# Optimization experiments

Hardware: AMD Instinct MI355X
Metric: run time of the kernel (lower is better)

## Reference

```python
import jax, jax.numpy as jnp
import numpy as np

N = 1024
DIM = 128
HEADS = 8
DK = DIM // HEADS
EDIM = 16
EPS = 1e-5
NEG = -10000.0


def _lin(k, din, dout):
    return jax.random.normal(k, (din, dout), jnp.float32) * (1.0 / np.sqrt(din))


def setup_inputs() -> dict:
    key = jax.random.key(0)
    ks = jax.random.split(key, 10)
    mask = jax.random.randint(ks[2], (N, N), 0, 2).astype(bool)
    mask = mask | jnp.eye(N, dtype=bool)  # self-loops always valid
    return {
        "x": jax.random.normal(ks[0], (N, DIM), jnp.float32),
        "edge_feat": jax.random.normal(ks[1], (N, N, EDIM), jnp.float32),
        "mask": mask,
        "Wq": _lin(ks[3], DIM, DIM), "bq": jnp.zeros((DIM,), jnp.float32),
        "Wk": _lin(ks[4], DIM, DIM), "bk": jnp.zeros((DIM,), jnp.float32),
        "Wv": _lin(ks[5], DIM, DIM), "bv": jnp.zeros((DIM,), jnp.float32),
        "Wae": _lin(ks[6], EDIM, HEADS), "bae": jnp.zeros((HEADS,), jnp.float32),
        "Wve": _lin(ks[7], EDIM, DIM), "bve": jnp.zeros((DIM,), jnp.float32),
        "Wo": _lin(ks[8], DIM, DIM), "bo": jnp.zeros((DIM,), jnp.float32),
        "gamma": jnp.ones((DIM,), jnp.float32),
        "beta": jnp.zeros((DIM,), jnp.float32),
    }


def reference(x, edge_feat, mask, Wq, bq, Wk, bk, Wv, bv, Wae, bae, Wve, bve, Wo, bo, gamma, beta):
    n, dim = x.shape
    heads = bae.shape[0]
    dk = dim // heads
    # pre-LayerNorm
    mu = jnp.mean(x, axis=-1, keepdims=True)
    var = jnp.mean(jnp.square(x - mu), axis=-1, keepdims=True)
    h = (x - mu) * jax.lax.rsqrt(var + EPS) * gamma + beta
    q = (h @ Wq + bq).reshape(n, heads, dk)
    k = (h @ Wk + bk).reshape(n, heads, dk)
    v = (h @ Wv + bv).reshape(n, heads, dk)
    # attention logits with per-edge additive bias: (n, m, heads)
    att = jnp.einsum('nhd,mhd->nmh', q, k) / np.sqrt(dk).astype(np.float32)
    att = att + edge_feat @ Wae + bae
    att = jnp.where(mask[..., None], att, NEG)
    alpha = jax.nn.softmax(att, axis=1)  # softmax over source nodes m
    # edge-conditioned values: msg_{nm} = v_m + U(e_{nm})
    edge_val = (edge_feat @ Wve + bve).reshape(n, n, heads, dk)
    out = jnp.einsum('nmh,mhd->nhd', alpha, v) + jnp.einsum('nmh,nmhd->nhd', alpha, edge_val)
    out = out.reshape(n, dim) @ Wo + bo
    return x + out
```

## Files before the change

### kernel.cpp

```cpp
#include <hip/hip_runtime.h>
#include <hip/hip_bf16.h>

#define NNODE 1024
#define DIM 128
#define HEADS 8
#define DK 16
#define EDIM 16
#define BN 8
#define NGRP 8
#define KV_ROW 160
#define H_STRIDE 20
#define EF_ROW 20
#define EFW_NSTR 104
#define LOG2E 1.44269504f

#define WREG 2176
#define VW_OFF 640
#define EFW_OFF 1280
#define MKW_OFF 2112
#define SMEM_F (4 * WREG)

__global__ __launch_bounds__(384)
void ln_qkv_kernel(const float* __restrict__ x,
                   const float* __restrict__ Wq, const float* __restrict__ bq,
                   const float* __restrict__ Wk, const float* __restrict__ bk,
                   const float* __restrict__ Wv, const float* __restrict__ bv,
                   const float* __restrict__ gamma, const float* __restrict__ beta,
                   float* __restrict__ qg, float* __restrict__ kg, float* __restrict__ vg) {
    const int n = blockIdx.x;
    const int t = threadIdx.x;
    __shared__ float hrow[DIM];
    __shared__ float part[4];

    float xv = 0.f;
    if (t < 128) {
        xv = x[n * DIM + t];
        float v = xv;
        #pragma unroll
        for (int off = 32; off >= 1; off >>= 1) v += __shfl_xor(v, off);
        if ((t & 63) == 0) part[t >> 6] = v;
    }
    __syncthreads();
    const float mu = (part[0] + part[1]) * (1.0f / DIM);
    const float dx = xv - mu;
    if (t < 128) {
        float v = dx * dx;
        #pragma unroll
        for (int off = 32; off >= 1; off >>= 1) v += __shfl_xor(v, off);
        if ((t & 63) == 0) part[2 + (t >> 6)] = v;
    }
    __syncthreads();
    if (t < 128) {
        const float var = (part[2] + part[3]) * (1.0f / DIM);
        hrow[t] = dx * rsqrtf(var + 1e-5f) * gamma[t] + beta[t];
    }
    __syncthreads();

    const int which = t >> 7;
    const int col = t & 127;
    const float* W = (which == 0) ? Wq : (which == 1) ? Wk : Wv;
    const float* b = (which == 0) ? bq : (which == 1) ? bk : bv;
    float* o       = (which == 0) ? qg : (which == 1) ? kg : vg;
    float a0 = b[col], a1 = 0.f;
    #pragma unroll 8
    for (int i = 0; i < DIM; i += 2) {
        a0 = fmaf(hrow[i],     W[i * DIM + col],       a0);
        a1 = fmaf(hrow[i + 1], W[(i + 1) * DIM + col], a1);
    }
    o[n * DIM + col] = a0 + a1;
}

__global__ __launch_bounds__(256, 2)
void attn_kernel(const float* __restrict__ qg, const float* __restrict__ kg,
                 const float* __restrict__ vg, const float* __restrict__ ef,
                 const int* __restrict__ mask,
                 const float* __restrict__ Wae, const float* __restrict__ bae,
                 float* __restrict__ acc) {
    const int t = threadIdx.x;
    const int lane = t & 63;
    const int wid = t >> 6;
    const int sp = lane >> 5;
    const int np = (lane >> 3) & 3;
    const int h  = lane & 7;
    const int bx = blockIdx.x;
    const int n0  = (bx >> 3) * BN;
    const int grp = bx & 7;
    const int mb_w = grp * 128 + wid * 32;

    __shared__ float smem[SMEM_F];
    float* k_w  = smem + wid * WREG;
    float* v_w  = k_w + VW_OFF;
    float* ef_w = k_w + EFW_OFF;
    int*   mk_w = (int*)(k_w + MKW_OFF);

    float qreg[2][DK];
    #pragma unroll
    for (int hf = 0; hf < 2; ++hf) {
        const float* qp = qg + (size_t)(n0 + np + 4 * hf) * DIM + h * DK;
        #pragma unroll
        for (int d4 = 0; d4 < 4; ++d4) {
            const float4 qv = *(const float4*)(qp + d4 * 4);
            qreg[hf][d4 * 4 + 0] = qv.x; qreg[hf][d4 * 4 + 1] = qv.y;
            qreg[hf][d4 * 4 + 2] = qv.z; qreg[hf][d4 * 4 + 3] = qv.w;
        }
    }
    float waec[EDIM];
    #pragma unroll
    for (int e = 0; e < EDIM; ++e) waec[e] = Wae[e * HEADS + h] * LOG2E;
    const float baeh = bae[h] * LOG2E;

    float sl[2] = {0.f, 0.f};
    float accv[2][DK], accT[2][EDIM];
    #pragma unroll
    for (int hf = 0; hf < 2; ++hf) {
        #pragma unroll
        for (int d = 0; d < DK; ++d) accv[hf][d] = 0.f;
        #pragma unroll
        for (int e = 0; e < EDIM; ++e) accT[hf][e] = 0.f;
    }

    #pragma unroll 1
    for (int c = 0; c < 8; ++c) {
        const int mb = mb_w + c * 4;

        const int kvrow = sp * 2 + (np >> 1);
        const int kvc4  = (np & 1) * 16 + (h << 1);
        float4 kq[2], vq[2], ev[2]; int mki = 0;
        #pragma unroll
        for (int r = 0; r < 2; ++r) {
            const int idx = r * 64 + lane;
            const int row = idx >> 5, c4 = idx & 31;
            kq[r] = *(const float4*)(kg + (size_t)(mb + row) * DIM + c4 * 4);
            vq[r] = *(const float4*)(vg + (size_t)(mb + row) * DIM + c4 * 4);
        }
        #pragma unroll
        for (int r = 0; r < 2; ++r) {
            const int idx = r * 64 + lane;
            const int nn = idx >> 4, mm = (idx >> 2) & 3, q4 = idx & 3;
            ev[r] = *(const float4*)(ef + ((size_t)(n0 + nn) * NNODE + mb + mm) * EDIM + q4 * 4);
        }
        if (lane < 32)
            mki = mask[(size_t)(n0 + (lane >> 2)) * NNODE + (mb + (lane & 3))];
        #pragma unroll
        for (int r = 0; r < 2; ++r) {
            const int idx = r * 64 + lane;
            const int row = idx >> 5, c4 = idx & 31;
            const int hh = c4 >> 2, d4 = c4 & 3;
            *(float4*)&k_w[row * KV_ROW + hh * H_STRIDE + d4 * 4] = kq[r];
            *(float4*)&v_w[row * KV_ROW + hh * H_STRIDE + d4 * 4] = vq[r];
        }
        #pragma unroll
        for (int r = 0; r < 2; ++r) {
            const int idx = r * 64 + lane;
            const int nn = idx >> 4, mm = (idx >> 2) & 3, q4 = idx & 3;
            *(float4*)&ef_w[nn * EFW_NSTR + mm * EF_ROW + q4 * 4] = ev[r];
        }
        if (lane < 32)
            mk_w[lane] = mki;

        #pragma unroll
        for (int j = 0; j < 2; ++j) {
            const int ml = sp * 2 + j;
            float kk[DK], vv[DK];
            const float* kp = &k_w[ml * KV_ROW + h * H_STRIDE];
            const float* vp = &v_w[ml * KV_ROW + h * H_STRIDE];
            #pragma unroll
            for (int d4 = 0; d4 < 4; ++d4) {
                const float4 k4 = *(const float4*)(kp + d4 * 4);
                kk[d4 * 4 + 0] = k4.x; kk[d4 * 4 + 1] = k4.y;
                kk[d4 * 4 + 2] = k4.z; kk[d4 * 4 + 3] = k4.w;
                const float4 v4 = *(const float4*)(vp + d4 * 4);
                vv[d4 * 4 + 0] = v4.x; vv[d4 * 4 + 1] = v4.y;
                vv[d4 * 4 + 2] = v4.z; vv[d4 * 4 + 3] = v4.w;
            }
            #pragma unroll
            for (int hf = 0; hf < 2; ++hf) {
                const int n = np + 4 * hf;
                const float* ep = &ef_w[n * EFW_NSTR + ml * EF_ROW];
                float efv[EDIM];
                #pragma unroll
                for (int e4 = 0; e4 < 4; ++e4) {
                    const float4 e4v = *(const float4*)(ep + e4 * 4);
                    efv[e4 * 4 + 0] = e4v.x; efv[e4 * 4 + 1] = e4v.y;
                    efv[e4 * 4 + 2] = e4v.z; efv[e4 * 4 + 3] = e4v.w;
                }
                float bias = baeh, dot = 0.f;
                #pragma unroll
                for (int e = 0; e < EDIM; ++e) bias = fmaf(efv[e], waec[e], bias);
                #pragma unroll
                for (int d = 0; d < DK; ++d) dot = fmaf(qreg[hf][d], kk[d], dot);
                const float lg = fmaf(dot, 0.25f * LOG2E, bias);
                const float p = mk_w[n * 4 + ml] ? __builtin_amdgcn_exp2f(lg) : 0.f;
                sl[hf] += p;
                #pragma unroll
                for (int d = 0; d < DK; ++d) accv[hf][d] = fmaf(p, vv[d], accv[hf][d]);
                #pragma unroll
                for (int e = 0; e < EDIM; ++e) accT[hf][e] = fmaf(p, efv[e], accT[hf][e]);
            }
        }
    }

    #pragma unroll
    for (int hf = 0; hf < 2; ++hf) {
        sl[hf] += __shfl_xor(sl[hf], 32);
        #pragma unroll
        for (int d = 0; d < DK; ++d) accv[hf][d] += __shfl_xor(accv[hf][d], 32);
        #pragma unroll
        for (int e = 0; e < EDIM; ++e) accT[hf][e] += __shfl_xor(accT[hf][e], 32);
    }
    __syncthreads();
    float* red = smem;
    if (lane < 32) {
        float* rp = &red[((wid * 4 + np) * 8 + h) * 66];
        #pragma unroll
        for (int hf = 0; hf < 2; ++hf) {
            rp[hf * 33 + 0] = sl[hf];
            #pragma unroll
            for (int d = 0; d < DK; ++d) rp[hf * 33 + 1 + d] = accv[hf][d];
            #pragma unroll
            for (int e = 0; e < EDIM; ++e) rp[hf * 33 + 17 + e] = accT[hf][e];
        }
    }
    __syncthreads();
    for (int v = t; v < BN * HEADS * 33; v += 256) {
        const int n = v / 264;
        const int rem = v - n * 264;
        const int hh = rem / 33;
        const int idx = rem - hh * 33;
        const int nnp = n & 3, hf = n >> 2;
        float sum = 0.f;
        #pragma unroll
        for (int w = 0; w < 4; ++w)
            sum += red[((w * 4 + nnp) * 8 + hh) * 66 + hf * 33 + idx];
        acc[((size_t)(n0 + n) * NGRP + grp) * 264 + rem] = sum;
    }
}

__global__ __launch_bounds__(128)
void final_kernel(const float* __restrict__ acc,
                  const float* __restrict__ Wve, const float* __restrict__ bve,
                  const float* __restrict__ x,
                  const float* __restrict__ Wo, const float* __restrict__ bo,
                  float* __restrict__ out) {
    const int n = blockIdx.x, t = threadIdx.x;
    __shared__ float ab[HEADS * 33];
    __shared__ float orow[DIM];
    const float* ap = acc + (size_t)n * NGRP * 264;
    for (int u = t; u < HEADS * 33; u += 128) {
        float sv = 0.f;
        #pragma unroll
        for (int g = 0; g < NGRP; ++g) sv += ap[g * 264 + u];
        ab[u] = sv;
    }
    __syncthreads();
    const int col = t, hh = col >> 4, dd = col & 15;
    const float slv = ab[hh * 33];
    float acc2 = 0.f;
    #pragma unroll
    for (int e = 0; e < EDIM; ++e) acc2 = fmaf(ab[hh * 33 + 17 + e], Wve[e * DIM + col], acc2);
    orow[col] = (ab[hh * 33 + 1 + dd] + acc2) / slv + bve[col];
    __syncthreads();
    float o0 = bo[col] + x[(size_t)n * DIM + col], o1 = 0.f;
    #pragma unroll 8
    for (int i = 0; i < DIM; i += 2) {
        o0 = fmaf(orow[i],     Wo[i * DIM + col],       o0);
        o1 = fmaf(orow[i + 1], Wo[(i + 1) * DIM + col], o1);
    }
    out[(size_t)n * DIM + col] = o0 + o1;
}

extern "C" void kernel_launch(void* const* d_in, const int* in_sizes, int n_in,
                              void* d_out, int out_size, void* d_ws, size_t ws_size,
                              hipStream_t stream) {
    const float* x     = (const float*)d_in[0];
    const float* ef    = (const float*)d_in[1];
    const int*   mask  = (const int*)d_in[2];
    const float* Wq    = (const float*)d_in[3];
    const float* bq    = (const float*)d_in[4];
    const float* Wk    = (const float*)d_in[5];
    const float* bk    = (const float*)d_in[6];
    const float* Wv    = (const float*)d_in[7];
    const float* bv    = (const float*)d_in[8];
    const float* Wae   = (const float*)d_in[9];
    const float* bae   = (const float*)d_in[10];
    const float* Wve   = (const float*)d_in[11];
    const float* bve   = (const float*)d_in[12];
    const float* Wo    = (const float*)d_in[13];
    const float* bo    = (const float*)d_in[14];
    const float* gamma = (const float*)d_in[15];
    const float* beta  = (const float*)d_in[16];

    float* ws = (float*)d_ws;
    float* accb = ws;
    float* qg   = ws + (size_t)NNODE * NGRP * 264;
    float* kg   = qg + (size_t)NNODE * DIM;
    float* vg   = kg + (size_t)NNODE * DIM;

    ln_qkv_kernel<<<NNODE, 384, 0, stream>>>(x, Wq, bq, Wk, bk, Wv, bv, gamma, beta, qg, kg, vg);
    attn_kernel<<<(NNODE / BN) * NGRP, 256, 0, stream>>>(qg, kg, vg, ef, mask, Wae, bae, accb);
    final_kernel<<<NNODE, 128, 0, stream>>>(accb, Wve, bve, x, Wo, bo, (float*)d_out);
}
```

Before: 172.6 us.

## Double-buffer edge features in LDS and read K/V/mask directly from global

Stops staging K, V and mask through shared memory each chunk and loads them straight from global memory (L1/L2-cached) into registers. Edge features are now double-buffered in LDS, with the next chunk's tile issued as a global load before compute and stored after it, so load latency overlaps the math. Launch bounds drop from 2 to 1 block per SIMD hint, giving the compiler more registers for the prefetch buffers at the cost of possibly lower occupancy. Warp-private buffers mean no barriers are needed, but redundant global K/V reads across lanes rely on cache hits.

```diff
diff --git a/kernel.cpp b/kernel.cpp
--- a/kernel.cpp
+++ b/kernel.cpp
@@ -8,17 +8,13 @@
 #define EDIM 16
 #define BN 8
 #define NGRP 8
-#define KV_ROW 160
-#define H_STRIDE 20
 #define EF_ROW 20
 #define EFW_NSTR 104
+#define EFB 832
+#define WREG 1664
 #define LOG2E 1.44269504f
 
-#define WREG 2176
-#define VW_OFF 640
-#define EFW_OFF 1280
-#define MKW_OFF 2112
-#define SMEM_F (4 * WREG)
+#define SMEM_F 8448
 
 __global__ __launch_bounds__(384)
 void ln_qkv_kernel(const float* __restrict__ x,
@@ -70,7 +66,7 @@
     o[n * DIM + col] = a0 + a1;
 }
 
-__global__ __launch_bounds__(256, 2)
+__global__ __launch_bounds__(256, 1)
 void attn_kernel(const float* __restrict__ qg, const float* __restrict__ kg,
                  const float* __restrict__ vg, const float* __restrict__ ef,
                  const int* __restrict__ mask,
@@ -88,10 +84,7 @@
     const int mb_w = grp * 128 + wid * 32;
 
     __shared__ float smem[SMEM_F];
-    float* k_w  = smem + wid * WREG;
-    float* v_w  = k_w + VW_OFF;
-    float* ef_w = k_w + EFW_OFF;
-    int*   mk_w = (int*)(k_w + MKW_OFF);
+    float* ef_w = smem + wid * WREG;
 
     float qreg[2][DK];
     #pragma unroll
@@ -119,51 +112,41 @@
         for (int e = 0; e < EDIM; ++e) accT[hf][e] = 0.f;
     }
 
+    #pragma unroll
+    for (int r = 0; r < 2; ++r) {
+        const int idx = r * 64 + lane;
+        const int nn = idx >> 4, mm = (idx >> 2) & 3, q4 = idx & 3;
+        const float4 ev0 = *(const float4*)(ef + ((size_t)(n0 + nn) * NNODE + mb_w + mm) * EDIM + q4 * 4);
+        *(float4*)&ef_w[nn * EFW_NSTR + mm * EF_ROW + q4 * 4] = ev0;
+    }
+
     #pragma unroll 1
     for (int c = 0; c < 8; ++c) {
         const int mb = mb_w + c * 4;
-
-        const int kvrow = sp * 2 + (np >> 1);
-        const int kvc4  = (np & 1) * 16 + (h << 1);
-        float4 kq[2], vq[2], ev[2]; int mki = 0;
-        #pragma unroll
-        for (int r = 0; r < 2; ++r) {
-            const int idx = r * 64 + lane;
-            const int row = idx >> 5, c4 = idx & 31;
-            kq[r] = *(const float4*)(kg + (size_t)(mb + row) * DIM + c4 * 4);
-            vq[r] = *(const float4*)(vg + (size_t)(mb + row) * DIM + c4 * 4);
-        }
-        #pragma unroll
-        for (int r = 0; r < 2; ++r) {
-            const int idx = r * 64 + lane;
-            const int nn = idx >> 4, mm = (idx >> 2) & 3, q4 = idx & 3;
-            ev[r] = *(const float4*)(ef + ((size_t)(n0 + nn) * NNODE + mb + mm) * EDIM + q4 * 4);
-        }
-        if (lane < 32)
-            mki = mask[(size_t)(n0 + (lane >> 2)) * NNODE + (mb + (lane & 3))];
-        #pragma unroll
-        for (int r = 0; r < 2; ++r) {
-            const int idx = r * 64 + lane;
-            const int row = idx >> 5, c4 = idx & 31;
-            const int hh = c4 >> 2, d4 = c4 & 3;
-            *(float4*)&k_w[row * KV_ROW + hh * H_STRIDE + d4 * 4] = kq[r];
-            *(float4*)&v_w[row * KV_ROW + hh * H_STRIDE + d4 * 4] = vq[r];
-        }
-        #pragma unroll
-        for (int r = 0; r < 2; ++r) {
-            const int idx = r * 64 + lane;
-            const int nn = idx >> 4, mm = (idx >> 2) & 3, q4 = idx & 3;
-            *(float4*)&ef_w[nn * EFW_NSTR + mm * EF_ROW + q4 * 4] = ev[r];
-        }
-        if (lane < 32)
-            mk_w[lane] = mki;
+        const float* efc = ef_w + (c & 1) * EFB;
+        const bool pf = (c < 7);
+
+        float4 ev[2];
+        if (pf) {
+            #pragma unroll
+            for (int r = 0; r < 2; ++r) {
+                const int idx = r * 64 + lane;
+                const int nn = idx >> 4, mm = (idx >> 2) & 3, q4 = idx & 3;
+                ev[r] = *(const float4*)(ef + ((size_t)(n0 + nn) * NNODE + (mb + 4) + mm) * EDIM + q4 * 4);
+            }
+        }
+
+        int2 mk[2];
+        #pragma unroll
+        for (int hf = 0; hf < 2; ++hf)
+            mk[hf] = *(const int2*)(mask + (size_t)(n0 + np + 4 * hf) * NNODE + mb + 2 * sp);
 
         #pragma unroll
         for (int j = 0; j < 2; ++j) {
             const int ml = sp * 2 + j;
             float kk[DK], vv[DK];
-            const float* kp = &k_w[ml * KV_ROW + h * H_STRIDE];
-            const float* vp = &v_w[ml * KV_ROW + h * H_STRIDE];
+            const float* kp = kg + (size_t)(mb + ml) * DIM + h * DK;
+            const float* vp = vg + (size_t)(mb + ml) * DIM + h * DK;
             #pragma unroll
             for (int d4 = 0; d4 < 4; ++d4) {
                 const float4 k4 = *(const float4*)(kp + d4 * 4);
@@ -176,7 +159,7 @@
             #pragma unroll
             for (int hf = 0; hf < 2; ++hf) {
                 const int n = np + 4 * hf;
-                const float* ep = &ef_w[n * EFW_NSTR + ml * EF_ROW];
+                const float* ep = &efc[n * EFW_NSTR + ml * EF_ROW];
                 float efv[EDIM];
                 #pragma unroll
                 for (int e4 = 0; e4 < 4; ++e4) {
@@ -190,12 +173,23 @@
                 #pragma unroll
                 for (int d = 0; d < DK; ++d) dot = fmaf(qreg[hf][d], kk[d], dot);
                 const float lg = fmaf(dot, 0.25f * LOG2E, bias);
-                const float p = mk_w[n * 4 + ml] ? __builtin_amdgcn_exp2f(lg) : 0.f;
+                const int mv = j ? mk[hf].y : mk[hf].x;
+                const float p = mv ? __builtin_amdgcn_exp2f(lg) : 0.f;
                 sl[hf] += p;
                 #pragma unroll
                 for (int d = 0; d < DK; ++d) accv[hf][d] = fmaf(p, vv[d], accv[hf][d]);
                 #pragma unroll
                 for (int e = 0; e < EDIM; ++e) accT[hf][e] = fmaf(p, efv[e], accT[hf][e]);
+            }
+        }
+
+        if (pf) {
+            float* efn = ef_w + ((c + 1) & 1) * EFB;
+            #pragma unroll
+            for (int r = 0; r < 2; ++r) {
+                const int idx = r * 64 + lane;
+                const int nn = idx >> 4, mm = (idx >> 2) & 3, q4 = idx & 3;
+                *(float4*)&efn[nn * EFW_NSTR + mm * EF_ROW + q4 * 4] = ev[r];
             }
         }
     }
```

After: 211.8 us. 22.7% more time.
